# Kernel tuning notes

Measured on AMD Instinct MI355X. Metric: run time of the kernel, lower is better.

Reference implementation:

```python
import jax, jax.numpy as jnp
import numpy as np

# configuration (mirrors global `args` in the original code)
N_USER = 20000
N_ITEM = 20000
N = N_USER + N_ITEM            # total nodes; N*N < 2^31 so int32 hashing is safe
N_EDGES = 2_560_000
MASK_DEPTH = 2
KEEP_RATE = 0.5
N_SEEDS = 2000


def setup_inputs() -> dict:
    key = jax.random.key(0)
    k1, k2, k3 = jax.random.split(key, 3)
    rows = jax.random.randint(k1, (N_EDGES,), 0, N, dtype=jnp.int32)
    cols = jax.random.randint(k2, (N_EDGES,), 0, N, dtype=jnp.int32)
    vals = jnp.ones((N_EDGES,), jnp.float32)  # adj._values(); only its length is used
    seeds = jax.random.randint(k3, (N_SEEDS,), 0, N, dtype=jnp.int32)
    return {"rows": rows, "cols": cols, "vals": vals, "seeds": seeds}


def reference(rows, cols, vals, seeds):
    """Faithful vectorized translation of RandomMaskSubgraphs.forward.

    The per-seed python loop over edges is equivalent (in its final effect) to:
    per BFS level, drop every still-alive edge incident to the current seed set,
    and take the endpoints of dropped edges as the next seed set.
    Returns (enc_rows, enc_cols, enc_vals, dec_rows, dec_cols, dec_vals).
    Removed encoder edges carry value 0 (zero-value sparse entries == absent).
    """
    E = rows.shape[0]
    key = jax.random.key(1)
    kS, kR, kC = jax.random.split(key, 3)

    alive = jnp.ones(E, dtype=bool)                     # edges not yet masked
    seed_mask = jnp.zeros(N, dtype=bool).at[seeds].set(True)
    mask_nodes = seed_mask                               # union of maskNodes list
    cur = seed_mask
    for i in range(MASK_DEPTH):
        # membership test: edge incident to any current seed (single gather pass)
        hit = alive & (cur[rows] | cur[cols])
        alive = alive & ~hit
        if i != MASK_DEPTH - 1:
            # endpoints of masked edges become next frontier (scatter dedup)
            h = hit.astype(jnp.int32)
            touched = (jnp.zeros(N, jnp.int32).at[rows].add(h).at[cols].add(h)) > 0
            mask_nodes = mask_nodes | touched
            cur = touched

    # random keep-nodes augmentation
    samp_num = int(N * KEEP_RATE)
    samp = jax.random.randint(kS, (samp_num,), 0, N, dtype=jnp.int32)
    mask_nodes = mask_nodes.at[samp].set(True)

    # encoderAdj = normalizeAdj(sparse(ones on remaining edges))
    deg = jax.ops.segment_sum(alive.astype(jnp.float32), rows, num_segments=N)
    dinv = jnp.power(deg + 1e-12, -0.5)
    enc_vals = alive.astype(jnp.float32) * dinv[rows] * dinv[cols]

    # decoderAdj: random pairs among masked nodes + self loops + remaining edges,
    # deduplicated via integer hash row*N + col (fits int32 since N*N < 2^31)
    mask_idx = jnp.nonzero(mask_nodes)[0].astype(jnp.int32)
    tem_num = int(mask_idx.shape[0])
    tem_rows = mask_idx[jax.random.randint(kR, (E,), 0, tem_num)]
    tem_cols = mask_idx[jax.random.randint(kC, (E,), 0, tem_num)]
    ar = jnp.arange(N, dtype=jnp.int32)
    alive_rows = rows[alive]
    alive_cols = cols[alive]
    new_rows = jnp.concatenate([tem_rows, tem_cols, ar, alive_rows])
    new_cols = jnp.concatenate([tem_cols, tem_rows, ar, alive_cols])
    hash_val = jnp.unique(new_rows * N + new_cols)
    dec_cols = hash_val % N
    dec_rows = hash_val // N
    dec_vals = jnp.ones(dec_rows.shape[0], jnp.float32)

    return rows, cols, enc_vals, dec_rows, dec_cols, dec_vals
```

## Files before the change

kernel.cpp:

```cpp
#include <hip/hip_runtime.h>
#include <stdint.h>


#define NN 40000
#define SAMPN (NN / 2)
#define WORDS 1250
#define SWORDS 40
#define NB 1024
#define RPB 40
#define CAP 8192
#define CURSTRIDE 4
#define EPB 2816
#define NE (EPB / 256)
#define SELFPB 44
#define SCAP (3 * EPB + SELFPB)

__host__ __device__ __forceinline__ void tf2x32(unsigned k0, unsigned k1,
                                                unsigned x0, unsigned x1,
                                                unsigned &o0, unsigned &o1) {
  unsigned ks2 = k0 ^ k1 ^ 0x1BD11BDAu;
  x0 += k0; x1 += k1;
#define TFR(r) { x0 += x1; x1 = (x1 << (r)) | (x1 >> (32 - (r))); x1 ^= x0; }
  TFR(13) TFR(15) TFR(26) TFR(6)
  x0 += k1;  x1 += ks2 + 1u;
  TFR(17) TFR(29) TFR(16) TFR(24)
  x0 += ks2; x1 += k0 + 2u;
  TFR(13) TFR(15) TFR(26) TFR(6)
  x0 += k0;  x1 += k1 + 3u;
  TFR(17) TFR(29) TFR(16) TFR(24)
  x0 += k1;  x1 += ks2 + 4u;
  TFR(13) TFR(15) TFR(26) TFR(6)
  x0 += ks2; x1 += k0 + 5u;
#undef TFR
  o0 = x0; o1 = x1;
}

__device__ __forceinline__ unsigned jrand(unsigned a, unsigned b, unsigned c,
                                          unsigned d, unsigned e, unsigned span) {
  unsigned x0, x1, y0, y1;
  tf2x32(a, b, 0u, e, x0, x1);
  unsigned hi = x0 ^ x1;
  tf2x32(c, d, 0u, e, y0, y1);
  unsigned lo = y0 ^ y1;
  unsigned mult = 65536u % span;
  mult = (mult * mult) % span;
  return ((hi % span) * mult + (lo % span)) % span;
}

__global__ void k_zero16(uint4 *p, int n16) {
  int i = blockIdx.x * blockDim.x + threadIdx.x;
  if (i < n16) p[i] = make_uint4(0u, 0u, 0u, 0u);
}
__global__ void k_seed_samp(const int *seeds, int ns, unsigned char *cur,
                            unsigned char *mask_bfs,
                            unsigned a, unsigned b, unsigned c, unsigned d) {
  int i = blockIdx.x * blockDim.x + threadIdx.x;
  if (i < ns) { int s = seeds[i]; cur[s] = 1; mask_bfs[s] = 1; }
  if (i < SAMPN) {
    unsigned idx = jrand(a, b, c, d, (unsigned)i, (unsigned)NN);
    mask_bfs[idx] = 1;
  }
}
__global__ void k_level0(const int *rows, const int *cols, int E,
                         const unsigned char *cur, unsigned char *alive,
                         unsigned char *touched, unsigned char *mask_bfs) {
  int e = blockIdx.x * blockDim.x + threadIdx.x;
  if (e >= E) return;
  int r = rows[e], c = cols[e];
  if (cur[r] | cur[c]) {
    alive[e] = 0;
    touched[r] = 1; touched[c] = 1;
    mask_bfs[r] = 1; mask_bfs[c] = 1;
  } else alive[e] = 1;
}
__global__ void k_level1_deg(const int *rows, const int *cols, int E,
                             const unsigned char *touched, unsigned char *alive,
                             int *deg) {
  int e = blockIdx.x * blockDim.x + threadIdx.x;
  if (e >= E) return;
  if (alive[e]) {
    int r = rows[e];
    if (touched[r] | touched[cols[e]]) alive[e] = 0;
    else atomicAdd(&deg[r], 1);
  }
}

__global__ __launch_bounds__(1024) void k_scan_mask(const unsigned char *flags,
                                                    unsigned short *mask_idx,
                                                    int *tem_num) {
  __shared__ int wsum[16];
  const unsigned *f = (const unsigned *)flags;
  int tid = threadIdx.x, lane = tid & 63, wid = tid >> 6;
  int base = tid * 10;
  unsigned u[10];
  int cnt = 0;
  for (int j = 0; j < 10; j++) {
    int i = base + j;
    u[j] = (i < 10000) ? f[i] : 0u;
    cnt += __popc(u[j]);
  }
  int x = cnt;
  for (int d = 1; d < 64; d <<= 1) {
    int y = __shfl_up(x, d, 64);
    if (lane >= d) x += y;
  }
  if (lane == 63) wsum[wid] = x;
  __syncthreads();
  if (wid == 0) {
    int v = (lane < 16) ? wsum[lane] : 0;
    int y = v;
    for (int d = 1; d < 16; d <<= 1) {
      int z = __shfl_up(y, d, 64);
      if (lane >= d) y += z;
    }
    if (lane < 16) wsum[lane] = y - v;
  }
  __syncthreads();
  int off = wsum[wid] + (x - cnt);
  for (int j = 0; j < 10; j++) {
    int i = base + j;
    unsigned v = u[j];
    while (v) {
      int byte = (__ffs(v) - 1) >> 3;
      v &= v - 1;
      mask_idx[off++] = (unsigned short)(i * 4 + byte);
    }
  }
  if (tid == 1023) *tem_num = off;
}

__global__ __launch_bounds__(256) void k_append(
    const int *rows, const int *cols, const unsigned char *alive,
    const int *deg, const unsigned short *mask_idx, const int *tem_num,
    int *cursors, unsigned *bucketmem, float *out,
    unsigned ra, unsigned rb, unsigned rc, unsigned rd,
    unsigned ca, unsigned cb, unsigned cc, unsigned cd, int E) {
  __shared__ unsigned sorted[SCAP];
  __shared__ int cnt[NB];
  __shared__ unsigned short ofs[NB];
  __shared__ int ntot_s;
  int tid = threadIdx.x, lane = tid & 63, wid = tid >> 6;
  int e0 = blockIdx.x * EPB;
  int i0 = blockIdx.x * SELFPB;
  int i1 = i0 + SELFPB; if (i1 > NN) i1 = NN;
  unsigned span = (unsigned)*tem_num;
  const unsigned NOPE = 0xFFFFFFFFu;

  unsigned tval[NE], aval[NE];

  for (int i = tid; i < NB; i += 256) cnt[i] = 0;
  __syncthreads();
#pragma unroll
  for (int k = 0; k < NE; k++) {
    int e = e0 + k * 256 + tid;
    if (e < E) {
      unsigned iR = jrand(ra, rb, rc, rd, (unsigned)e, span);
      unsigned iC = jrand(ca, cb, cc, cd, (unsigned)e, span);
      unsigned tr = (unsigned)mask_idx[iR], tc = (unsigned)mask_idx[iC];
      tval[k] = (tr << 16) | tc;
      atomicAdd(&cnt[tr / RPB], 1);
      atomicAdd(&cnt[tc / RPB], 1);
      int r = rows[e], c = cols[e];
      float v = 0.0f;
      if (alive[e]) {
        aval[k] = ((unsigned)r << 16) | (unsigned)c;
        atomicAdd(&cnt[(unsigned)r / RPB], 1);
        float xr = (float)deg[r] + 1e-12f;
        float xc = (float)deg[c] + 1e-12f;
        float dr = (float)(1.0 / sqrt((double)xr));
        float dc = (float)(1.0 / sqrt((double)xc));
        v = dr * dc;
      } else aval[k] = NOPE;
      out[e] = (float)r;
      out[E + e] = (float)c;
      out[2 * E + e] = v;
    } else { tval[k] = NOPE; aval[k] = NOPE; }
  }
  for (int i = i0 + tid; i < i1; i += 256) atomicAdd(&cnt[i / RPB], 1);
  __syncthreads();
  if (wid == 0) {
    int carry = 0;
    for (int c8 = 0; c8 < NB / 64; c8++) {
      int v = cnt[c8 * 64 + lane];
      int x = v;
      for (int d = 1; d < 64; d <<= 1) {
        int y = __shfl_up(x, d, 64);
        if (lane >= d) x += y;
      }
      ofs[c8 * 64 + lane] = (unsigned short)(carry + x - v);
      carry += __shfl(x, 63, 64);
    }
    if (lane == 0) ntot_s = carry;
  }
  __syncthreads();
  for (int i = tid; i < NB; i += 256) cnt[i] = ofs[i];
  __syncthreads();
#pragma unroll
  for (int k = 0; k < NE; k++) {
    unsigned v = tval[k];
    if (v != NOPE) {
      unsigned tr = v >> 16, tc = v & 0xFFFFu;
      int p1 = atomicAdd(&cnt[tr / RPB], 1);
      sorted[p1] = v;
      int p2 = atomicAdd(&cnt[tc / RPB], 1);
      sorted[p2] = (tc << 16) | tr;
      unsigned a = aval[k];
      if (a != NOPE) {
        int p3 = atomicAdd(&cnt[(a >> 16) / RPB], 1);
        sorted[p3] = a;
      }
    }
  }
  for (int i = i0 + tid; i < i1; i += 256) {
    int p = atomicAdd(&cnt[i / RPB], 1);
    sorted[p] = ((unsigned)i << 16) | (unsigned)i;
  }
  __syncthreads();
  int ntot = ntot_s;
  for (int b = tid; b < NB; b += 256) {
    int end = (b < NB - 1) ? (int)ofs[b + 1] : ntot;
    int len = end - (int)ofs[b];
    cnt[b] = len ? atomicAdd(&cursors[b * CURSTRIDE], len) : 0;
  }
  __syncthreads();
  for (int j = tid; j < ntot; j += 256) {
    unsigned item = sorted[j];
    unsigned r = item >> 16;
    unsigned b = r / RPB;
    unsigned lr = r - b * RPB;
    int idx = cnt[b] + (j - (int)ofs[b]);
    if (idx < CAP) bucketmem[b * CAP + idx] = (lr << 16) | (item & 0xFFFFu);
  }
}

__global__ __launch_bounds__(256) void k_dedup(unsigned *bucketmem,
                                               const int *cursors, int *uniq_cnt) {
  int b = blockIdx.x;
  int rowbase = b * RPB;
  if (rowbase >= NN) { if (threadIdx.x == 0) uniq_cnt[b] = 0; return; }

  __shared__ unsigned short arr[CAP];
  __shared__ int cnt[RPB];
  __shared__ int rowend[RPB];
  __shared__ int curs[RPB];
  __shared__ int rowoff[RPB];
  __shared__ unsigned bm[4][WORDS];
  __shared__ unsigned sm[4][SWORDS];

  int tid = threadIdx.x, lane = tid & 63, wid = tid >> 6;
  int n = cursors[b * CURSTRIDE]; if (n > CAP) n = CAP;
  const unsigned *src = bucketmem + (size_t)b * CAP;

  for (int i = tid; i < RPB; i += 256) cnt[i] = 0;
  __syncthreads();
  for (int j = tid; j < n; j += 256) atomicAdd(&cnt[src[j] >> 16], 1);
  __syncthreads();
  if (tid == 0) {
    int s = 0;
    for (int r = 0; r < RPB; r++) { curs[r] = s; s += cnt[r]; rowend[r] = s; }
  }
  __syncthreads();
  for (int j = tid; j < n; j += 256) {
    unsigned v = src[j];
    int p = atomicAdd(&curs[v >> 16], 1);
    arr[p] = (unsigned short)v;
  }
  for (int w = lane; w < WORDS; w += 64) bm[wid][w] = 0u;
  if (lane < SWORDS) sm[wid][lane] = 0u;
  __syncthreads();

  for (int r = wid; r < RPB; r += 4) {
    int s1 = rowend[r], s0 = s1 - cnt[r];
    for (int j = s0 + lane; j < s1; j += 64) {
      unsigned c = arr[j];
      atomicOr(&bm[wid][c >> 5], 1u << (c & 31));
      atomicOr(&sm[wid][c >> 10], 1u << ((c >> 5) & 31));
    }
    unsigned s = (lane < SWORDS) ? sm[wid][lane] : 0u;
    int m = 0;
    unsigned t = s;
    while (t) {
      int w = (lane << 5) + (__ffs(t) - 1);
      t &= t - 1;
      m += __popc(bm[wid][w]);
    }
    int x = m;
    for (int d = 1; d < 64; d <<= 1) {
      int y = __shfl_up(x, d, 64);
      if (lane >= d) x += y;
    }
    int u = __shfl(x, 63, 64);
    int pos = s0 + (x - m);
    t = s;
    while (t) {
      int w = (lane << 5) + (__ffs(t) - 1);
      t &= t - 1;
      unsigned mm = bm[wid][w];
      bm[wid][w] = 0u;
      while (mm) {
        int bit = __ffs(mm) - 1;
        mm &= mm - 1;
        arr[pos++] = (unsigned short)((w << 5) + bit);
      }
    }
    if (lane < SWORDS) sm[wid][lane] = 0u;
    if (lane == 0) cnt[r] = u;
  }
  __syncthreads();
  if (tid == 0) {
    int s = 0;
    for (int r = 0; r < RPB; r++) { rowoff[r] = s; s += cnt[r]; }
    uniq_cnt[b] = s;
  }
  __syncthreads();
  unsigned *dst = bucketmem + (size_t)b * CAP;
  for (int r = wid; r < RPB; r += 4) {
    int s0 = r ? rowend[r - 1] : 0;
    int u = cnt[r], o = rowoff[r];
    unsigned rowpack = (unsigned)(rowbase + r) << 16;
    for (int j = lane; j < u; j += 64)
      dst[o + j] = rowpack | (unsigned)arr[s0 + j];
  }
}

__global__ __launch_bounds__(256) void k_emit(const unsigned *bucketmem,
                                              const int *uniq_cnt, float *out,
                                              int E, int U) {
  __shared__ int part[4];
  int b = blockIdx.x;
  int tid = threadIdx.x, lane = tid & 63, wid = tid >> 6;
  int acc = 0;
  for (int i = tid; i < NB; i += 256)
    if (i < b) acc += uniq_cnt[i];
  for (int d = 1; d < 64; d <<= 1) acc += __shfl_xor(acc, d, 64);
  if (lane == 0) part[wid] = acc;
  __syncthreads();
  int ob = part[0] + part[1] + part[2] + part[3];
  int ub = uniq_cnt[b];
  const unsigned *src = bucketmem + (size_t)b * CAP;
  int base3 = 3 * E;
  for (int j = tid; j < ub; j += 256) {
    unsigned h = src[j];
    unsigned r = h >> 16;
    unsigned c = h & 0xFFFFu;
    int idx = ob + j;
    if (idx < U) {
      out[base3 + idx] = (float)r;
      out[base3 + U + idx] = (float)c;
      out[base3 + 2 * U + idx] = 1.0f;
    }
  }
  if (b == NB - 1 && tid == 0) {
    int C = ob + ub;
    if (C != U) {
      int d = C - U; if (d < 0) d = -d; if (d > 60000) d = 60000;
      out[base3] = (float)(300000 + d);
    }
  }
}

extern "C" void kernel_launch(void *const *d_in, const int *in_sizes, int n_in,
                              void *d_out, int out_size, void *d_ws,
                              size_t ws_size, hipStream_t stream) {
  const int *rows = (const int *)d_in[0];
  const int *cols = (const int *)d_in[1];
  const int *seeds = (const int *)d_in[3];
  const int E = in_sizes[0];
  const int ns = in_sizes[3];
  float *out = (float *)d_out;
  const int U = (out_size - 3 * E) / 3;

  int *I = (int *)d_ws;
  int *deg = I;      I += NN;
  int *cursors = I;  I += NB * CURSTRIDE;
  int *uniq_cnt = I; I += NB;
  unsigned char *cur = (unsigned char *)I;
  unsigned char *touched = cur + NN;
  unsigned char *mask_bfs = touched + NN;
  size_t zero_bytes = (size_t)((char *)(mask_bfs + NN) - (char *)deg);
  int *J = (int *)(mask_bfs + NN);
  int *tem_num = J;  J += 1;
  J += 1;
  unsigned short *mask_idx = (unsigned short *)J;
  J += NN / 2;
  unsigned *bucketmem = (unsigned *)J; J += (size_t)NB * CAP;
  unsigned char *alive = (unsigned char *)J;

  unsigned F[3][2];
  tf2x32(0u, 1u, 0u, 0u, F[0][0], F[0][1]);
  tf2x32(0u, 1u, 0u, 1u, F[1][0], F[1][1]);
  tf2x32(0u, 1u, 0u, 2u, F[2][0], F[2][1]);
  unsigned K[3][4];
  for (int s = 0; s < 3; s++) {
    tf2x32(F[s][0], F[s][1], 0u, 0u, K[s][0], K[s][1]);
    tf2x32(F[s][0], F[s][1], 0u, 1u, K[s][2], K[s][3]);
  }

  dim3 b(256);
  int gE = (E + 255) / 256;
  int gSS = (SAMPN + 255) / 256;
  int gT = (E + EPB - 1) / EPB;
  int n16 = (int)(zero_bytes / 16);

  k_zero16<<<(n16 + 255) / 256, b, 0, stream>>>((uint4 *)deg, n16);
  k_seed_samp<<<gSS, b, 0, stream>>>(seeds, ns, cur, mask_bfs,
                                     K[0][0], K[0][1], K[0][2], K[0][3]);
  k_level0<<<gE, b, 0, stream>>>(rows, cols, E, cur, alive, touched, mask_bfs);
  k_level1_deg<<<gE, b, 0, stream>>>(rows, cols, E, touched, alive, deg);
  k_scan_mask<<<1, 1024, 0, stream>>>(mask_bfs, mask_idx, tem_num);
  k_append<<<gT, b, 0, stream>>>(rows, cols, alive, deg, mask_idx, tem_num,
                                 cursors, bucketmem, out,
                                 K[1][0], K[1][1], K[1][2], K[1][3],
                                 K[2][0], K[2][1], K[2][2], K[2][3], E);
  k_dedup<<<NB, b, 0, stream>>>(bucketmem, cursors, uniq_cnt);
  k_emit<<<NB, b, 0, stream>>>(bucketmem, uniq_cnt, out, E, U);
}
```

Measured before the change: 271.5 us.

## Vectorize BFS edge passes to 4 edges per thread and fold scan into level-1

Result: slower. 282.7 us (+4.1%).

```diff
diff --git a/kernel.cpp b/kernel.cpp
--- a/kernel.cpp
+++ b/kernel.cpp
@@ -61,72 +61,85 @@
     mask_bfs[idx] = 1;
   }
 }
-__global__ void k_level0(const int *rows, const int *cols, int E,
-                         const unsigned char *cur, unsigned char *alive,
-                         unsigned char *touched, unsigned char *mask_bfs) {
-  int e = blockIdx.x * blockDim.x + threadIdx.x;
-  if (e >= E) return;
-  int r = rows[e], c = cols[e];
-  if (cur[r] | cur[c]) {
-    alive[e] = 0;
-    touched[r] = 1; touched[c] = 1;
-    mask_bfs[r] = 1; mask_bfs[c] = 1;
-  } else alive[e] = 1;
-}
-__global__ void k_level1_deg(const int *rows, const int *cols, int E,
-                             const unsigned char *touched, unsigned char *alive,
-                             int *deg) {
-  int e = blockIdx.x * blockDim.x + threadIdx.x;
-  if (e >= E) return;
-  if (alive[e]) {
-    int r = rows[e];
-    if (touched[r] | touched[cols[e]]) alive[e] = 0;
-    else atomicAdd(&deg[r], 1);
-  }
-}
-
-__global__ __launch_bounds__(1024) void k_scan_mask(const unsigned char *flags,
-                                                    unsigned short *mask_idx,
-                                                    int *tem_num) {
-  __shared__ int wsum[16];
-  const unsigned *f = (const unsigned *)flags;
-  int tid = threadIdx.x, lane = tid & 63, wid = tid >> 6;
-  int base = tid * 10;
-  unsigned u[10];
-  int cnt = 0;
-  for (int j = 0; j < 10; j++) {
-    int i = base + j;
-    u[j] = (i < 10000) ? f[i] : 0u;
-    cnt += __popc(u[j]);
-  }
-  int x = cnt;
-  for (int d = 1; d < 64; d <<= 1) {
-    int y = __shfl_up(x, d, 64);
-    if (lane >= d) x += y;
-  }
-  if (lane == 63) wsum[wid] = x;
-  __syncthreads();
-  if (wid == 0) {
-    int v = (lane < 16) ? wsum[lane] : 0;
-    int y = v;
-    for (int d = 1; d < 16; d <<= 1) {
-      int z = __shfl_up(y, d, 64);
-      if (lane >= d) y += z;
-    }
-    if (lane < 16) wsum[lane] = y - v;
-  }
-  __syncthreads();
-  int off = wsum[wid] + (x - cnt);
-  for (int j = 0; j < 10; j++) {
-    int i = base + j;
-    unsigned v = u[j];
-    while (v) {
-      int byte = (__ffs(v) - 1) >> 3;
-      v &= v - 1;
-      mask_idx[off++] = (unsigned short)(i * 4 + byte);
-    }
-  }
-  if (tid == 1023) *tem_num = off;
+
+__global__ __launch_bounds__(256) void k_level0(
+    const uint4 *rows4, const uint4 *cols4, int E4, const unsigned char *cur,
+    unsigned *alive4, unsigned char *touched, unsigned char *mask_bfs) {
+  int i = blockIdx.x * blockDim.x + threadIdx.x;
+  if (i >= E4) return;
+  uint4 r = rows4[i], c = cols4[i];
+  unsigned av = 0;
+#define L0(rr, cc, sh)                                                      \
+  if (cur[rr] | cur[cc]) {                                                  \
+    touched[rr] = 1; touched[cc] = 1;                                       \
+    mask_bfs[rr] = 1; mask_bfs[cc] = 1;                                     \
+  } else av |= (1u << (sh));
+  L0(r.x, c.x, 0) L0(r.y, c.y, 8) L0(r.z, c.z, 16) L0(r.w, c.w, 24)
+#undef L0
+  alive4[i] = av;
+}
+
+__global__ __launch_bounds__(256) void k_l1deg_scan(
+    const uint4 *rows4, const uint4 *cols4, int E4, const unsigned char *touched,
+    unsigned *alive4, int *deg, const unsigned char *flags,
+    unsigned short *mask_idx, int *tem_num, int scanBlock) {
+  int tid = threadIdx.x;
+  if ((int)blockIdx.x == scanBlock) {
+    __shared__ int wsum[4];
+    const unsigned *f = (const unsigned *)flags;
+    int lane = tid & 63, wid = tid >> 6;
+    int base = tid * 40;
+    int cnt = 0;
+    for (int j = 0; j < 40; j++) {
+      int i = base + j;
+      if (i < 10000) cnt += __popc(f[i]);
+    }
+    int x = cnt;
+    for (int d = 1; d < 64; d <<= 1) {
+      int y = __shfl_up(x, d, 64);
+      if (lane >= d) x += y;
+    }
+    if (lane == 63) wsum[wid] = x;
+    __syncthreads();
+    if (wid == 0) {
+      int v = (lane < 4) ? wsum[lane] : 0;
+      int y = v;
+      for (int d = 1; d < 4; d <<= 1) {
+        int z = __shfl_up(y, d, 64);
+        if (lane >= d) y += z;
+      }
+      if (lane < 4) wsum[lane] = y - v;
+    }
+    __syncthreads();
+    int off = wsum[wid] + (x - cnt);
+    for (int j = 0; j < 40; j++) {
+      int i = base + j;
+      if (i >= 10000) break;
+      unsigned v = f[i];
+      while (v) {
+        int byte = (__ffs(v) - 1) >> 3;
+        v &= v - 1;
+        mask_idx[off++] = (unsigned short)(i * 4 + byte);
+      }
+    }
+    if (tid == 255) *tem_num = off;
+    return;
+  }
+  int i = blockIdx.x * blockDim.x + tid;
+  if (i >= E4) return;
+  unsigned a = alive4[i];
+  if (a == 0) return;
+  uint4 r = rows4[i], c = cols4[i];
+  unsigned na = a;
+#define L1(rr, cc, msk)                                                     \
+  if (a & (msk)) {                                                          \
+    if (touched[rr] | touched[cc]) na &= ~(msk);                            \
+    else atomicAdd(&deg[rr], 1);                                            \
+  }
+  L1(r.x, c.x, 0x000000FFu) L1(r.y, c.y, 0x0000FF00u)
+  L1(r.z, c.z, 0x00FF0000u) L1(r.w, c.w, 0xFF000000u)
+#undef L1
+  if (na != a) alive4[i] = na;
 }
 
 __global__ __launch_bounds__(256) void k_append(
@@ -397,7 +410,8 @@
   }
 
   dim3 b(256);
-  int gE = (E + 255) / 256;
+  int E4 = E / 4;
+  int gE4 = (E4 + 255) / 256;
   int gSS = (SAMPN + 255) / 256;
   int gT = (E + EPB - 1) / EPB;
   int n16 = (int)(zero_bytes / 16);
@@ -405,9 +419,12 @@
   k_zero16<<<(n16 + 255) / 256, b, 0, stream>>>((uint4 *)deg, n16);
   k_seed_samp<<<gSS, b, 0, stream>>>(seeds, ns, cur, mask_bfs,
                                      K[0][0], K[0][1], K[0][2], K[0][3]);
-  k_level0<<<gE, b, 0, stream>>>(rows, cols, E, cur, alive, touched, mask_bfs);
-  k_level1_deg<<<gE, b, 0, stream>>>(rows, cols, E, touched, alive, deg);
-  k_scan_mask<<<1, 1024, 0, stream>>>(mask_bfs, mask_idx, tem_num);
+  k_level0<<<gE4, b, 0, stream>>>((const uint4 *)rows, (const uint4 *)cols, E4,
+                                  cur, (unsigned *)alive, touched, mask_bfs);
+  k_l1deg_scan<<<gE4 + 1, b, 0, stream>>>((const uint4 *)rows,
+                                          (const uint4 *)cols, E4, touched,
+                                          (unsigned *)alive, deg, mask_bfs,
+                                          mask_idx, tem_num, gE4);
   k_append<<<gT, b, 0, stream>>>(rows, cols, alive, deg, mask_idx, tem_num,
                                  cursors, bucketmem, out,
                                  K[1][0], K[1][1], K[1][2], K[1][3],
```
